# Kernel tuning notes

Measured on AMD Instinct MI355X. Metric: run time of the kernel, lower is better.

The kernel has to match this reference:

```python
import jax, jax.numpy as jnp
import numpy as np

N_NODES = 50000
N_EDGES = 800000
N_GRAPHS = 2048
F = 78  # num_features_xd


def gcn_conv(x, src, dst, W, b):
    """PyG GCNConv: x' = D^{-1/2}(A+I)D^{-1/2} (x W) + b, self-loops added."""
    n = x.shape[0]
    xw = x @ W  # dense transform first (PyG order)
    loop = jnp.arange(n)
    s = jnp.concatenate([src, loop])
    d = jnp.concatenate([dst, loop])
    deg = jax.ops.segment_sum(jnp.ones(d.shape[0], dtype=xw.dtype), d, num_segments=n)
    dis = jnp.where(deg > 0, jax.lax.rsqrt(deg), 0.0)
    norm = dis[s] * dis[d]  # [E+N]
    msg = xw[s] * norm[:, None]  # gather + scale, [E+N, Fout]
    out = jax.ops.segment_sum(msg, d, num_segments=n)  # scatter-add to targets
    return out + b


def setup_inputs() -> dict:
    key = jax.random.key(0)
    ks = jax.random.split(key, 9)

    def glorot(k, shape):
        lim = float(np.sqrt(6.0 / (shape[0] + shape[1])))
        return jax.random.uniform(k, shape, minval=-lim, maxval=lim, dtype=jnp.float32)

    x = jax.random.normal(ks[0], (N_NODES, F), dtype=jnp.float32)
    edge_index = jax.random.randint(ks[1], (2, N_EDGES), 0, N_NODES, dtype=jnp.int64)
    batch = jnp.sort(jax.random.randint(ks[2], (N_NODES,), 0, N_GRAPHS, dtype=jnp.int64))
    drug2 = jax.random.normal(ks[3], (N_GRAPHS, 489), dtype=jnp.float32)

    W1 = glorot(ks[4], (F, F));        b1 = jnp.zeros((F,), jnp.float32)
    W2 = glorot(ks[5], (F, 2 * F));    b2 = jnp.zeros((2 * F,), jnp.float32)
    W3 = glorot(ks[6], (2 * F, 4 * F)); b3 = jnp.zeros((4 * F,), jnp.float32)
    Wfc = glorot(ks[7], (4 * F, 489)); bfc = jnp.zeros((489,), jnp.float32)

    return dict(x=x, edge_index=edge_index, batch=batch, drug2=drug2,
                W1=W1, b1=b1, W2=W2, b2=b2, W3=W3, b3=b3, Wfc=Wfc, bfc=bfc)


def reference(x, edge_index, batch, drug2, W1, b1, W2, b2, W3, b3, Wfc, bfc):
    src, dst = edge_index[0], edge_index[1]
    h = jax.nn.relu(gcn_conv(x, src, dst, W1, b1))   # dropout = identity (eval mode)
    h = jax.nn.relu(gcn_conv(h, src, dst, W2, b2))
    h = jax.nn.relu(gcn_conv(h, src, dst, W3, b3))
    g = jax.ops.segment_max(h, batch, num_segments=N_GRAPHS)  # global max pool
    g = jnp.where(jnp.isfinite(g), g, 0.0)  # guard empty graphs
    g = jax.nn.relu(g @ Wfc + bfc)
    return g + drug2
```

## Files before the change

kernel.cpp:

```cpp
#include <hip/hip_runtime.h>

#define NNODES 50000
#define NEDGES 800000
#define NGRAPHS 2048

typedef __attribute__((ext_vector_type(8))) short bf16x8;
typedef __attribute__((ext_vector_type(4))) float f32x4;

__device__ __forceinline__ float bf2f(ushort u) {
    return __uint_as_float(((uint)u) << 16);
}
__device__ __forceinline__ ushort f2bf(float f) {
    uint u = __float_as_uint(f);
    return (ushort)((u + 0x7fff + ((u >> 16) & 1)) >> 16);
}

__global__ void deg_count(const int* __restrict__ dst, int* __restrict__ cnt, int E) {
    int e = blockIdx.x * blockDim.x + threadIdx.x;
    if (e < E) atomicAdd(&cnt[dst[e]], 1);
}

__global__ void block_scan(const int* __restrict__ cnt, int* __restrict__ lp,
                           int* __restrict__ bsum, int M) {
    __shared__ int s[256];
    int t = threadIdx.x;
    int n = blockIdx.x * 256 + t;
    int v = (n < M) ? cnt[n] : 0;
    s[t] = v;
    __syncthreads();
    #pragma unroll
    for (int off = 1; off < 256; off <<= 1) {
        int u = (t >= off) ? s[t - off] : 0;
        __syncthreads();
        s[t] += u;
        __syncthreads();
    }
    if (n < M) lp[n] = s[t] - v;
    if (t == 255) bsum[blockIdx.x] = s[255];
}

__global__ void scan_bsum(int* __restrict__ bsum, int NB) {
    __shared__ int s[256];
    int t = threadIdx.x;
    int v = (t < NB) ? bsum[t] : 0;
    s[t] = v;
    __syncthreads();
    #pragma unroll
    for (int off = 1; off < 256; off <<= 1) {
        int u = (t >= off) ? s[t - off] : 0;
        __syncthreads();
        s[t] += u;
        __syncthreads();
    }
    if (t < NB) bsum[t] = s[t] - v;
}

__global__ void finalize_rowptr(int* __restrict__ rowptr, int* __restrict__ cursor,
                                const int* __restrict__ bsum, const int* __restrict__ cnt,
                                float* __restrict__ dis,
                                const int* __restrict__ batch, int* __restrict__ gstart,
                                int M, int E, int G) {
    int n = blockIdx.x * blockDim.x + threadIdx.x;
    if (n < M) {
        int v = rowptr[n] + bsum[n >> 8];
        rowptr[n] = v;
        cursor[n] = v;
        dis[n] = rsqrtf((float)(cnt[n] + 1));
        int b = batch[n];
        int bp = (n == 0) ? -1 : batch[n - 1];
        for (int gg = bp + 1; gg <= b; ++gg) gstart[gg] = n;
        if (n == M - 1) {
            for (int gg = b + 1; gg <= G; ++gg) gstart[gg] = M;
        }
    }
    if (n == 0) rowptr[M] = E;
}

__global__ void fill_csr(const int* __restrict__ src, const int* __restrict__ dst,
                         const float* __restrict__ dis, int* __restrict__ cursor,
                         int2* __restrict__ csr, int E) {
    int e = blockIdx.x * blockDim.x + threadIdx.x;
    if (e >= E) return;
    int s = src[e], d = dst[e];
    int pos = atomicAdd(&cursor[d], 1);
    csr[pos] = make_int2(s, __float_as_int(dis[s] * dis[d]));
}

__global__ void prep_all(const float* __restrict__ x, ushort* __restrict__ xb,
                         const float* __restrict__ W1, ushort* __restrict__ W1t,
                         const float* __restrict__ W2, ushort* __restrict__ W2t,
                         const float* __restrict__ W3, ushort* __restrict__ W3t,
                         const float* __restrict__ Wfc, ushort* __restrict__ Wfct) {
    const int M = NNODES;
    const int KX = 80, F1 = 78, F2 = 156, F3 = 312, FC = 489;
    const int n0 = M * KX;
    const int n1 = 80 * 96, n2 = 160 * 96, n3 = 320 * 160, n4 = 496 * 320;
    int idx = blockIdx.x * blockDim.x + threadIdx.x;
    if (idx < n0) {
        int n = idx / KX, k = idx % KX;
        xb[idx] = (k < F1) ? f2bf(x[(size_t)n * F1 + k]) : (ushort)0;
        return;
    }
    idx -= n0;
    if (idx < n1) {
        int n = idx / 96, k = idx % 96;
        W1t[idx] = (k < F1 && n < F1) ? f2bf(W1[(size_t)k * F1 + n]) : (ushort)0;
        return;
    }
    idx -= n1;
    if (idx < n2) {
        int n = idx / 96, k = idx % 96;
        W2t[idx] = (k < F1 && n < F2) ? f2bf(W2[(size_t)k * F2 + n]) : (ushort)0;
        return;
    }
    idx -= n2;
    if (idx < n3) {
        int n = idx / 160, k = idx % 160;
        W3t[idx] = (k < F2 && n < F3) ? f2bf(W3[(size_t)k * F3 + n]) : (ushort)0;
        return;
    }
    idx -= n3;
    if (idx < n4) {
        int n = idx / 320, k = idx % 320;
        Wfct[idx] = (k < F3 && n < FC) ? f2bf(Wfc[(size_t)k * FC + n]) : (ushort)0;
    }
}

__device__ __forceinline__ void acc8(float* acc, uint4 v, float nm) {
    acc[0] += bf2f((ushort)(v.x & 0xffff)) * nm;
    acc[1] += bf2f((ushort)(v.x >> 16)) * nm;
    acc[2] += bf2f((ushort)(v.y & 0xffff)) * nm;
    acc[3] += bf2f((ushort)(v.y >> 16)) * nm;
    acc[4] += bf2f((ushort)(v.z & 0xffff)) * nm;
    acc[5] += bf2f((ushort)(v.z >> 16)) * nm;
    acc[6] += bf2f((ushort)(v.w & 0xffff)) * nm;
    acc[7] += bf2f((ushort)(v.w >> 16)) * nm;
}

template <int CH, int STR, int SUB, int CHOUT>
__global__ __launch_bounds__(128) void gather_ilp(const uint4* __restrict__ h,
                                                  const int* __restrict__ rowptr,
                                                  const int2* __restrict__ csr,
                                                  const float* __restrict__ dis,
                                                  uint4* __restrict__ agg) {
    int node = blockIdx.x * 2 + (threadIdx.x >> 6);
    if (node >= NNODES) return;
    int lane = threadIdx.x & 63;
    int sub = lane / CH;
    int ch = lane % CH;
    bool active = sub < SUB;

    float acc[8] = {};
    int beg = rowptr[node], end = rowptr[node + 1];
    for (int i = beg; i < end; i += 4 * SUB) {
        int2 ev[4];
        int vld[4];
        #pragma unroll
        for (int u = 0; u < 4; ++u) {
            int e = i + u * SUB + sub;
            vld[u] = active && (e < end);
            ev[u] = vld[u] ? csr[e] : make_int2(0, 0);
        }
        uint4 av[4];
        #pragma unroll
        for (int u = 0; u < 4; ++u)
            av[u] = vld[u] ? h[(size_t)ev[u].x * STR + ch] : make_uint4(0, 0, 0, 0);
        #pragma unroll
        for (int u = 0; u < 4; ++u)
            acc8(acc, av[u], __int_as_float(ev[u].y));
    }

    float tot[8];
    #pragma unroll
    for (int j = 0; j < 8; ++j) tot[j] = acc[j];
    #pragma unroll
    for (int sb = 1; sb < SUB; ++sb) {
        int srcLane = ch + sb * CH;
        #pragma unroll
        for (int j = 0; j < 8; ++j) tot[j] += __shfl(acc[j], srcLane);
    }

    if (lane < CHOUT) {
        uint4 o = make_uint4(0, 0, 0, 0);
        if (lane < CH) {
            float di = dis[node];
            float d2 = di * di;
            uint4 hs = h[(size_t)node * STR + lane];
            tot[0] += bf2f((ushort)(hs.x & 0xffff)) * d2;
            tot[1] += bf2f((ushort)(hs.x >> 16)) * d2;
            tot[2] += bf2f((ushort)(hs.y & 0xffff)) * d2;
            tot[3] += bf2f((ushort)(hs.y >> 16)) * d2;
            tot[4] += bf2f((ushort)(hs.z & 0xffff)) * d2;
            tot[5] += bf2f((ushort)(hs.z >> 16)) * d2;
            tot[6] += bf2f((ushort)(hs.w & 0xffff)) * d2;
            tot[7] += bf2f((ushort)(hs.w >> 16)) * d2;
            o.x = (uint)f2bf(tot[0]) | ((uint)f2bf(tot[1]) << 16);
            o.y = (uint)f2bf(tot[2]) | ((uint)f2bf(tot[3]) << 16);
            o.z = (uint)f2bf(tot[4]) | ((uint)f2bf(tot[5]) << 16);
            o.w = (uint)f2bf(tot[6]) | ((uint)f2bf(tot[7]) << 16);
        }
        agg[(size_t)node * CHOUT + lane] = o;
    }
}

template <int EPI>
__global__ __launch_bounds__(256) void gemm_mfma(const ushort* __restrict__ A,
                                                 const ushort* __restrict__ Bt,
                                                 ushort* __restrict__ Cb,
                                                 float* __restrict__ Cf,
                                                 const float* __restrict__ bias,
                                                 const float* __restrict__ addend,
                                                 int M, int Kp, int Np, int Nreal, int Cld) {
    __shared__ ushort Asl[64 * 32];
    __shared__ ushort Bsl[64 * 32];
    const int tid = threadIdx.x;
    const int lane = tid & 63;
    const int wid = tid >> 6;
    const int wm = (wid >> 1) * 32, wn = (wid & 1) * 32;
    const int bm = blockIdx.x * 64, bn = blockIdx.y * 64;

    const int sr = tid >> 2;
    const int sc = tid & 3;
    const int swz = sc ^ ((sr >> 1) & 3);
    const int lc = lane >> 4;

    f32x4 acc[2][2] = {};
    for (int k0 = 0; k0 < Kp; k0 += 32) {
        bf16x8 av = {};
        int gr = bm + sr;
        if (gr < M) av = *(const bf16x8*)&A[(size_t)gr * Kp + k0 + sc * 8];
        *(bf16x8*)&Asl[sr * 32 + swz * 8] = av;
        bf16x8 bv = {};
        int gn = bn + sr;
        if (gn < Np) bv = *(const bf16x8*)&Bt[(size_t)gn * Kp + k0 + sc * 8];
        *(bf16x8*)&Bsl[sr * 32 + swz * 8] = bv;
        __syncthreads();
        bf16x8 af[2], bfr[2];
        #pragma unroll
        for (int m = 0; m < 2; ++m) {
            int r = wm + m * 16 + (lane & 15);
            int pc = lc ^ ((r >> 1) & 3);
            af[m] = *(const bf16x8*)&Asl[r * 32 + pc * 8];
        }
        #pragma unroll
        for (int n = 0; n < 2; ++n) {
            int r = wn + n * 16 + (lane & 15);
            int pc = lc ^ ((r >> 1) & 3);
            bfr[n] = *(const bf16x8*)&Bsl[r * 32 + pc * 8];
        }
        #pragma unroll
        for (int m = 0; m < 2; ++m)
            #pragma unroll
            for (int n = 0; n < 2; ++n)
                acc[m][n] = __builtin_amdgcn_mfma_f32_16x16x32_bf16(af[m], bfr[n], acc[m][n], 0, 0, 0);
        __syncthreads();
    }
    #pragma unroll
    for (int m = 0; m < 2; ++m) {
        #pragma unroll
        for (int n = 0; n < 2; ++n) {
            int gc = bn + wn + n * 16 + (lane & 15);
            #pragma unroll
            for (int j = 0; j < 4; ++j) {
                int gr = bm + wm + m * 16 + (lane >> 4) * 4 + j;
                if (gr >= M) continue;
                float v = acc[m][n][j];
                if (EPI == 0) {
                    if (gc < Np) {
                        float o = (gc < Nreal) ? fmaxf(v + bias[gc], 0.f) : 0.f;
                        Cb[(size_t)gr * Cld + gc] = f2bf(o);
                    }
                } else {
                    if (gc < Nreal) {
                        float o = fmaxf(v + bias[gc], 0.f) + addend[(size_t)gr * Nreal + gc];
                        Cf[(size_t)gr * Nreal + gc] = o;
                    }
                }
            }
        }
    }
}

__global__ void pool_max_seg(const uint* __restrict__ h3, const int* __restrict__ gstart,
                             uint* __restrict__ gb, int PAIRS) {
    int g = blockIdx.x;
    int s = gstart[g], e = gstart[g + 1];
    for (int p = threadIdx.x; p < PAIRS; p += blockDim.x) {
        float mL = 0.f, mH = 0.f;
        for (int n = s; n < e; ++n) {
            uint v = h3[(size_t)n * PAIRS + p];
            mL = fmaxf(mL, bf2f((ushort)(v & 0xffff)));
            mH = fmaxf(mH, bf2f((ushort)(v >> 16)));
        }
        gb[(size_t)g * PAIRS + p] = (uint)f2bf(mL) | ((uint)f2bf(mH) << 16);
    }
}

extern "C" void kernel_launch(void* const* d_in, const int* in_sizes, int n_in,
                              void* d_out, int out_size, void* d_ws, size_t ws_size,
                              hipStream_t stream) {
    const float* x     = (const float*)d_in[0];
    const int*   eidx  = (const int*)d_in[1];
    const int*   batch = (const int*)d_in[2];
    const float* drug2 = (const float*)d_in[3];
    const float* W1 = (const float*)d_in[4];
    const float* b1 = (const float*)d_in[5];
    const float* W2 = (const float*)d_in[6];
    const float* b2 = (const float*)d_in[7];
    const float* W3 = (const float*)d_in[8];
    const float* b3 = (const float*)d_in[9];
    const float* Wfc = (const float*)d_in[10];
    const float* bfc = (const float*)d_in[11];
    float* out = (float*)d_out;

    const int M = NNODES, E = NEDGES, G = NGRAPHS;
    const int F1 = 78, F2 = 156, F3 = 312, FC = 489;
    const int Kx = 80;
    const int Kp1 = 96, Np1 = 80;
    const int Kp2 = 96, Np2 = 160;
    const int Kp3 = 160, Np3 = 320;
    const int Kpf = 320, Npf = 496;
    const int S2 = 192;

    const int* src = eidx;
    const int* dst = eidx + E;
    const int NB = (M + 255) / 256;

    char* ws = (char*)d_ws;
    size_t off = 0;
    auto alloc = [&](size_t bytes) {
        void* p = ws + off;
        off += (bytes + 255) & ~(size_t)255;
        return p;
    };
    ushort* xb   = (ushort*)alloc((size_t)M * Kx * 2);
    ushort* h1   = (ushort*)alloc((size_t)M * Np1 * 2);
    ushort* h2   = (ushort*)alloc((size_t)M * S2 * 2);
    ushort* h3   = (ushort*)alloc((size_t)M * Np3 * 2);
    ushort* agg  = (ushort*)alloc((size_t)M * Kp3 * 2);
    ushort* W1t  = (ushort*)alloc((size_t)Np1 * Kp1 * 2);
    ushort* W2t  = (ushort*)alloc((size_t)Np2 * Kp2 * 2);
    ushort* W3t  = (ushort*)alloc((size_t)Np3 * Kp3 * 2);
    ushort* Wfct = (ushort*)alloc((size_t)Npf * Kpf * 2);
    ushort* gb   = (ushort*)alloc((size_t)G * Kpf * 2);
    float* dis    = (float*)alloc((size_t)M * 4);
    int*   cnt    = (int*)alloc((size_t)M * 4);
    int*   rowptr = (int*)alloc((size_t)(M + 1) * 4);
    int*   cursor = (int*)alloc((size_t)M * 4);
    int*   bsum   = (int*)alloc(1024);
    int2*  csr    = (int2*)alloc((size_t)E * 8);
    int*   gstart  = (int*)alloc((size_t)(G + 1) * 4);

    hipMemsetAsync(cnt, 0, (size_t)M * 4, stream);
    deg_count<<<(E + 255) / 256, 256, 0, stream>>>(dst, cnt, E);
    block_scan<<<NB, 256, 0, stream>>>(cnt, rowptr, bsum, M);
    scan_bsum<<<1, 256, 0, stream>>>(bsum, NB);
    finalize_rowptr<<<NB, 256, 0, stream>>>(rowptr, cursor, bsum, cnt, dis, batch, gstart, M, E, G);
    fill_csr<<<(E + 255) / 256, 256, 0, stream>>>(src, dst, dis, cursor, csr, E);

    {
        int total = M * Kx + 80 * 96 + 160 * 96 + 320 * 160 + 496 * 320;
        prep_all<<<(total + 255) / 256, 256, 0, stream>>>(x, xb, W1, W1t, W2, W2t, W3, W3t, Wfc, Wfct);
    }

    const int GG = (M + 1) / 2;
    const int GMX = (M + 63) / 64;

    gather_ilp<10, 10, 6, 12><<<GG, 128, 0, stream>>>((const uint4*)xb, rowptr, csr, dis, (uint4*)agg);
    gemm_mfma<0><<<dim3(GMX, (Np1 + 63) / 64), 256, 0, stream>>>(agg, W1t, h1, nullptr, b1, nullptr, M, Kp1, Np1, F1, Np1);

    gather_ilp<10, 10, 6, 12><<<GG, 128, 0, stream>>>((const uint4*)h1, rowptr, csr, dis, (uint4*)agg);
    gemm_mfma<0><<<dim3(GMX, (Np2 + 63) / 64), 256, 0, stream>>>(agg, W2t, h2, nullptr, b2, nullptr, M, Kp2, Np2, F2, S2);

    gather_ilp<20, 24, 3, 20><<<GG, 128, 0, stream>>>((const uint4*)h2, rowptr, csr, dis, (uint4*)agg);
    gemm_mfma<0><<<dim3(GMX, Np3 / 64), 256, 0, stream>>>(agg, W3t, h3, nullptr, b3, nullptr, M, Kp3, Np3, F3, Np3);

    pool_max_seg<<<G, 256, 0, stream>>>((const uint*)h3, gstart, (uint*)gb, Kpf / 2);

    gemm_mfma<1><<<dim3((G + 63) / 64, (Npf + 63) / 64), 256, 0, stream>>>(gb, Wfct, nullptr, out, bfc, drug2, G, Kpf, Npf, FC, 0);
}
```

Measured before the change: 285.3 us.

## Build CSR via two-level bucket sort and compute edge norms on the fly

Replaces the global-atomic degree count, three-kernel scan and atomic CSR fill with a chunked histogram, bucket scan, shared-memory staged scatter into 256-node buckets, and a per-bucket local counting sort that also writes rowptr and dis. The CSR now stores only source indices, and the gather recomputes the edge norm from dis[src]*dis[node], which halves index traffic but adds a random dis load per edge. It also folds the graph-start computation into the prep kernel and shrinks the h2 row stride from 192 to 160. The point is to reduce global atomic contention and the number of small launches in graph preprocessing. Buckets above the shared capacity fall back to direct global writes.

```diff
diff --git a/kernel.cpp b/kernel.cpp
--- a/kernel.cpp
+++ b/kernel.cpp
@@ -3,6 +3,10 @@
 #define NNODES 50000
 #define NEDGES 800000
 #define NGRAPHS 2048
+#define CHUNK 4096
+#define NCHUNK ((NEDGES + CHUNK - 1) / CHUNK)
+#define NBUCK ((NNODES + 255) / 256)
+#define BCAP 4600
 
 typedef __attribute__((ext_vector_type(8))) short bf16x8;
 typedef __attribute__((ext_vector_type(4))) float f32x4;
@@ -15,82 +19,136 @@
     return (ushort)((u + 0x7fff + ((u >> 16) & 1)) >> 16);
 }
 
-__global__ void deg_count(const int* __restrict__ dst, int* __restrict__ cnt, int E) {
-    int e = blockIdx.x * blockDim.x + threadIdx.x;
-    if (e < E) atomicAdd(&cnt[dst[e]], 1);
-}
-
-__global__ void block_scan(const int* __restrict__ cnt, int* __restrict__ lp,
-                           int* __restrict__ bsum, int M) {
-    __shared__ int s[256];
+__global__ __launch_bounds__(256) void hist_pass(const int* __restrict__ dst,
+                                                 int* __restrict__ blockhist) {
+    __shared__ int bins[NBUCK];
+    int blk = blockIdx.x;
+    for (int i = threadIdx.x; i < NBUCK; i += 256) bins[i] = 0;
+    __syncthreads();
+    int e0 = blk * CHUNK;
+    int e1 = min(e0 + CHUNK, NEDGES);
+    for (int e = e0 + threadIdx.x; e < e1; e += 256)
+        atomicAdd(&bins[dst[e] >> 8], 1);
+    __syncthreads();
+    for (int i = threadIdx.x; i < NBUCK; i += 256)
+        blockhist[blk * NBUCK + i] = bins[i];
+}
+
+__global__ void bucket_scan(const int* __restrict__ blockhist,
+                            int* __restrict__ bucket_base,
+                            int* __restrict__ bucket_cursor) {
+    __shared__ int size_s[NBUCK];
+    for (int b = threadIdx.x; b < NBUCK; b += 256) {
+        int s = 0;
+        for (int c = 0; c < NCHUNK; ++c) s += blockhist[c * NBUCK + b];
+        size_s[b] = s;
+    }
+    __syncthreads();
+    if (threadIdx.x == 0) {
+        int run = 0;
+        for (int b = 0; b < NBUCK; ++b) { int v = size_s[b]; size_s[b] = run; run += v; }
+    }
+    __syncthreads();
+    for (int b = threadIdx.x; b < NBUCK; b += 256) {
+        bucket_base[b] = size_s[b];
+        bucket_cursor[b] = size_s[b];
+    }
+    if (threadIdx.x == 0) bucket_base[NBUCK] = NEDGES;
+}
+
+__global__ __launch_bounds__(256) void scatter_pass(const int* __restrict__ src,
+                                                    const int* __restrict__ dst,
+                                                    int* __restrict__ bucket_cursor,
+                                                    int2* __restrict__ ebuf) {
+    __shared__ int bins[NBUCK];
+    __shared__ int loff[NBUCK];
+    __shared__ int gbase[NBUCK];
+    __shared__ int lcur[NBUCK];
+    __shared__ int2 stage[CHUNK];
+    __shared__ int gaddr[CHUNK];
+    int blk = blockIdx.x;
+    int e0 = blk * CHUNK;
+    int e1 = min(e0 + CHUNK, NEDGES);
+    for (int i = threadIdx.x; i < NBUCK; i += 256) { bins[i] = 0; lcur[i] = 0; }
+    __syncthreads();
+    for (int e = e0 + threadIdx.x; e < e1; e += 256)
+        atomicAdd(&bins[dst[e] >> 8], 1);
+    __syncthreads();
+    if (threadIdx.x == 0) {
+        int run = 0;
+        for (int b = 0; b < NBUCK; ++b) { loff[b] = run; run += bins[b]; }
+    }
+    __syncthreads();
+    for (int b = threadIdx.x; b < NBUCK; b += 256)
+        gbase[b] = bins[b] ? atomicAdd(&bucket_cursor[b], bins[b]) : 0;
+    __syncthreads();
+    for (int e = e0 + threadIdx.x; e < e1; e += 256) {
+        int d = dst[e];
+        int b = d >> 8;
+        int p = atomicAdd(&lcur[b], 1);
+        int slot = loff[b] + p;
+        stage[slot] = make_int2(src[e], d);
+        gaddr[slot] = gbase[b] + p;
+    }
+    __syncthreads();
+    int cnt = e1 - e0;
+    for (int i = threadIdx.x; i < cnt; i += 256)
+        ebuf[gaddr[i]] = stage[i];
+}
+
+__global__ __launch_bounds__(256) void bucket_sort(const int2* __restrict__ ebuf,
+                                                   const int* __restrict__ bucket_base,
+                                                   int* __restrict__ csr_src,
+                                                   int* __restrict__ rowptr,
+                                                   float* __restrict__ dis) {
+    __shared__ int h[256], sc[257], cur[256];
+    __shared__ int srcstage[BCAP];
+    int b = blockIdx.x;
+    int base = bucket_base[b];
+    int cnt = bucket_base[b + 1] - base;
     int t = threadIdx.x;
-    int n = blockIdx.x * 256 + t;
-    int v = (n < M) ? cnt[n] : 0;
-    s[t] = v;
-    __syncthreads();
-    #pragma unroll
-    for (int off = 1; off < 256; off <<= 1) {
-        int u = (t >= off) ? s[t - off] : 0;
+    h[t] = 0;
+    cur[t] = 0;
+    __syncthreads();
+    for (int i = t; i < cnt; i += 256)
+        atomicAdd(&h[ebuf[base + i].y & 255], 1);
+    __syncthreads();
+    if (t == 0) {
+        int run = 0;
+        for (int j = 0; j < 256; ++j) { sc[j] = run; run += h[j]; }
+        sc[256] = run;
+    }
+    __syncthreads();
+    int node = b * 256 + t;
+    if (node <= NNODES) rowptr[node] = base + sc[t];
+    if (node < NNODES) dis[node] = rsqrtf((float)(h[t] + 1));
+    __syncthreads();
+    if (cnt <= BCAP) {
+        for (int i = t; i < cnt; i += 256) {
+            int2 r = ebuf[base + i];
+            int j = r.y & 255;
+            int p = atomicAdd(&cur[j], 1);
+            srcstage[sc[j] + p] = r.x;
+        }
         __syncthreads();
-        s[t] += u;
-        __syncthreads();
-    }
-    if (n < M) lp[n] = s[t] - v;
-    if (t == 255) bsum[blockIdx.x] = s[255];
-}
-
-__global__ void scan_bsum(int* __restrict__ bsum, int NB) {
-    __shared__ int s[256];
-    int t = threadIdx.x;
-    int v = (t < NB) ? bsum[t] : 0;
-    s[t] = v;
-    __syncthreads();
-    #pragma unroll
-    for (int off = 1; off < 256; off <<= 1) {
-        int u = (t >= off) ? s[t - off] : 0;
-        __syncthreads();
-        s[t] += u;
-        __syncthreads();
-    }
-    if (t < NB) bsum[t] = s[t] - v;
-}
-
-__global__ void finalize_rowptr(int* __restrict__ rowptr, int* __restrict__ cursor,
-                                const int* __restrict__ bsum, const int* __restrict__ cnt,
-                                float* __restrict__ dis,
-                                const int* __restrict__ batch, int* __restrict__ gstart,
-                                int M, int E, int G) {
-    int n = blockIdx.x * blockDim.x + threadIdx.x;
-    if (n < M) {
-        int v = rowptr[n] + bsum[n >> 8];
-        rowptr[n] = v;
-        cursor[n] = v;
-        dis[n] = rsqrtf((float)(cnt[n] + 1));
-        int b = batch[n];
-        int bp = (n == 0) ? -1 : batch[n - 1];
-        for (int gg = bp + 1; gg <= b; ++gg) gstart[gg] = n;
-        if (n == M - 1) {
-            for (int gg = b + 1; gg <= G; ++gg) gstart[gg] = M;
-        }
-    }
-    if (n == 0) rowptr[M] = E;
-}
-
-__global__ void fill_csr(const int* __restrict__ src, const int* __restrict__ dst,
-                         const float* __restrict__ dis, int* __restrict__ cursor,
-                         int2* __restrict__ csr, int E) {
-    int e = blockIdx.x * blockDim.x + threadIdx.x;
-    if (e >= E) return;
-    int s = src[e], d = dst[e];
-    int pos = atomicAdd(&cursor[d], 1);
-    csr[pos] = make_int2(s, __float_as_int(dis[s] * dis[d]));
+        for (int i = t; i < cnt; i += 256)
+            csr_src[base + i] = srcstage[i];
+    } else {
+        for (int i = t; i < cnt; i += 256) {
+            int2 r = ebuf[base + i];
+            int j = r.y & 255;
+            int p = atomicAdd(&cur[j], 1);
+            csr_src[base + sc[j] + p] = r.x;
+        }
+    }
 }
 
 __global__ void prep_all(const float* __restrict__ x, ushort* __restrict__ xb,
                          const float* __restrict__ W1, ushort* __restrict__ W1t,
                          const float* __restrict__ W2, ushort* __restrict__ W2t,
                          const float* __restrict__ W3, ushort* __restrict__ W3t,
-                         const float* __restrict__ Wfc, ushort* __restrict__ Wfct) {
+                         const float* __restrict__ Wfc, ushort* __restrict__ Wfct,
+                         const int* __restrict__ batch, int* __restrict__ gstart) {
     const int M = NNODES;
     const int KX = 80, F1 = 78, F2 = 156, F3 = 312, FC = 489;
     const int n0 = M * KX;
@@ -123,6 +181,17 @@
     if (idx < n4) {
         int n = idx / 320, k = idx % 320;
         Wfct[idx] = (k < F3 && n < FC) ? f2bf(Wfc[(size_t)k * FC + n]) : (ushort)0;
+        return;
+    }
+    idx -= n4;
+    if (idx < M) {
+        int n = idx;
+        int b = batch[n];
+        int bp = (n == 0) ? -1 : batch[n - 1];
+        for (int gg = bp + 1; gg <= b; ++gg) gstart[gg] = n;
+        if (n == M - 1) {
+            for (int gg = b + 1; gg <= NGRAPHS; ++gg) gstart[gg] = M;
+        }
     }
 }
 
@@ -140,7 +209,7 @@
 template <int CH, int STR, int SUB, int CHOUT>
 __global__ __launch_bounds__(128) void gather_ilp(const uint4* __restrict__ h,
                                                   const int* __restrict__ rowptr,
-                                                  const int2* __restrict__ csr,
+                                                  const int* __restrict__ csr_src,
                                                   const float* __restrict__ dis,
                                                   uint4* __restrict__ agg) {
     int node = blockIdx.x * 2 + (threadIdx.x >> 6);
@@ -149,25 +218,29 @@
     int sub = lane / CH;
     int ch = lane % CH;
     bool active = sub < SUB;
+    float di = dis[node];
 
     float acc[8] = {};
     int beg = rowptr[node], end = rowptr[node + 1];
     for (int i = beg; i < end; i += 4 * SUB) {
-        int2 ev[4];
+        int sidx[4];
         int vld[4];
         #pragma unroll
         for (int u = 0; u < 4; ++u) {
             int e = i + u * SUB + sub;
             vld[u] = active && (e < end);
-            ev[u] = vld[u] ? csr[e] : make_int2(0, 0);
+            sidx[u] = vld[u] ? csr_src[e] : 0;
         }
         uint4 av[4];
+        float ds[4];
+        #pragma unroll
+        for (int u = 0; u < 4; ++u) {
+            av[u] = vld[u] ? h[(size_t)sidx[u] * STR + ch] : make_uint4(0, 0, 0, 0);
+            ds[u] = dis[sidx[u]];
+        }
         #pragma unroll
         for (int u = 0; u < 4; ++u)
-            av[u] = vld[u] ? h[(size_t)ev[u].x * STR + ch] : make_uint4(0, 0, 0, 0);
-        #pragma unroll
-        for (int u = 0; u < 4; ++u)
-            acc8(acc, av[u], __int_as_float(ev[u].y));
+            acc8(acc, av[u], ds[u] * di);
     }
 
     float tot[8];
@@ -183,7 +256,6 @@
     if (lane < CHOUT) {
         uint4 o = make_uint4(0, 0, 0, 0);
         if (lane < CH) {
-            float di = dis[node];
             float d2 = di * di;
             uint4 hs = h[(size_t)node * STR + lane];
             tot[0] += bf2f((ushort)(hs.x & 0xffff)) * d2;
@@ -320,11 +392,9 @@
     const int Kp2 = 96, Np2 = 160;
     const int Kp3 = 160, Np3 = 320;
     const int Kpf = 320, Npf = 496;
-    const int S2 = 192;
 
     const int* src = eidx;
     const int* dst = eidx + E;
-    const int NB = (M + 255) / 256;
 
     char* ws = (char*)d_ws;
     size_t off = 0;
@@ -335,7 +405,7 @@
     };
     ushort* xb   = (ushort*)alloc((size_t)M * Kx * 2);
     ushort* h1   = (ushort*)alloc((size_t)M * Np1 * 2);
-    ushort* h2   = (ushort*)alloc((size_t)M * S2 * 2);
+    ushort* h2   = (ushort*)alloc((size_t)M * Np2 * 2);
     ushort* h3   = (ushort*)alloc((size_t)M * Np3 * 2);
     ushort* agg  = (ushort*)alloc((size_t)M * Kp3 * 2);
     ushort* W1t  = (ushort*)alloc((size_t)Np1 * Kp1 * 2);
@@ -344,38 +414,39 @@
     ushort* Wfct = (ushort*)alloc((size_t)Npf * Kpf * 2);
     ushort* gb   = (ushort*)alloc((size_t)G * Kpf * 2);
     float* dis    = (float*)alloc((size_t)M * 4);
-    int*   cnt    = (int*)alloc((size_t)M * 4);
     int*   rowptr = (int*)alloc((size_t)(M + 1) * 4);
-    int*   cursor = (int*)alloc((size_t)M * 4);
-    int*   bsum   = (int*)alloc(1024);
-    int2*  csr    = (int2*)alloc((size_t)E * 8);
-    int*   gstart  = (int*)alloc((size_t)(G + 1) * 4);
-
-    hipMemsetAsync(cnt, 0, (size_t)M * 4, stream);
-    deg_count<<<(E + 255) / 256, 256, 0, stream>>>(dst, cnt, E);
-    block_scan<<<NB, 256, 0, stream>>>(cnt, rowptr, bsum, M);
-    scan_bsum<<<1, 256, 0, stream>>>(bsum, NB);
-    finalize_rowptr<<<NB, 256, 0, stream>>>(rowptr, cursor, bsum, cnt, dis, batch, gstart, M, E, G);
-    fill_csr<<<(E + 255) / 256, 256, 0, stream>>>(src, dst, dis, cursor, csr, E);
+    int2*  ebuf   = (int2*)alloc((size_t)E * 8);
+    int*   csr_src = (int*)alloc((size_t)E * 4);
+    int*   blockhist = (int*)alloc((size_t)NCHUNK * NBUCK * 4);
+    int*   bucket_base = (int*)alloc((size_t)(NBUCK + 1) * 4);
+    int*   bucket_cursor = (int*)alloc((size_t)NBUCK * 4);
+    int*   gstart = (int*)alloc((size_t)(G + 1) * 4);
 
     {
-        int total = M * Kx + 80 * 96 + 160 * 96 + 320 * 160 + 496 * 320;
-        prep_all<<<(total + 255) / 256, 256, 0, stream>>>(x, xb, W1, W1t, W2, W2t, W3, W3t, Wfc, Wfct);
-    }
+        int total = M * Kx + 80 * 96 + 160 * 96 + 320 * 160 + 496 * 320 + M;
+        prep_all<<<(total + 255) / 256, 256, 0, stream>>>(
+            x, xb, W1, W1t, W2, W2t, W3, W3t, Wfc, Wfct, batch, gstart);
+    }
+
+    hist_pass<<<NCHUNK, 256, 0, stream>>>(dst, blockhist);
+    bucket_scan<<<1, 256, 0, stream>>>(blockhist, bucket_base, bucket_cursor);
+    scatter_pass<<<NCHUNK, 256, 0, stream>>>(src, dst, bucket_cursor, ebuf);
+    bucket_sort<<<NBUCK, 256, 0, stream>>>(ebuf, bucket_base, csr_src, rowptr, dis);
 
     const int GG = (M + 1) / 2;
     const int GMX = (M + 63) / 64;
 
-    gather_ilp<10, 10, 6, 12><<<GG, 128, 0, stream>>>((const uint4*)xb, rowptr, csr, dis, (uint4*)agg);
+    gather_ilp<10, 10, 6, 12><<<GG, 128, 0, stream>>>((const uint4*)xb, rowptr, csr_src, dis, (uint4*)agg);
     gemm_mfma<0><<<dim3(GMX, (Np1 + 63) / 64), 256, 0, stream>>>(agg, W1t, h1, nullptr, b1, nullptr, M, Kp1, Np1, F1, Np1);
 
-    gather_ilp<10, 10, 6, 12><<<GG, 128, 0, stream>>>((const uint4*)h1, rowptr, csr, dis, (uint4*)agg);
-    gemm_mfma<0><<<dim3(GMX, (Np2 + 63) / 64), 256, 0, stream>>>(agg, W2t, h2, nullptr, b2, nullptr, M, Kp2, Np2, F2, S2);
-
-    gather_ilp<20, 24, 3, 20><<<GG, 128, 0, stream>>>((const uint4*)h2, rowptr, csr, dis, (uint4*)agg);
+    gather_ilp<10, 10, 6, 12><<<GG, 128, 0, stream>>>((const uint4*)h1, rowptr, csr_src, dis, (uint4*)agg);
+    gemm_mfma<0><<<dim3(GMX, (Np2 + 63) / 64), 256, 0, stream>>>(agg, W2t, h2, nullptr, b2, nullptr, M, Kp2, Np2, F2, Np2);
+
+    gather_ilp<20, 20, 3, 20><<<GG, 128, 0, stream>>>((const uint4*)h2, rowptr, csr_src, dis, (uint4*)agg);
     gemm_mfma<0><<<dim3(GMX, Np3 / 64), 256, 0, stream>>>(agg, W3t, h3, nullptr, b3, nullptr, M, Kp3, Np3, F3, Np3);
 
     pool_max_seg<<<G, 256, 0, stream>>>((const uint*)h3, gstart, (uint*)gb, Kpf / 2);
 
-    gemm_mfma<1><<<dim3((G + 63) / 64, (Npf + 63) / 64), 256, 0, stream>>>(gb, Wfct, nullptr, out, bfc, drug2, G, Kpf, Npf, FC, 0);
-}
+    gemm_mfma<1><<<dim3((G + 63) / 64, (Npf + 63) / 64), 256, 0, stream>>>(
+        gb, Wfct, nullptr, out, bfc, drug2, G, Kpf, Npf, FC, 0);
+}
```

Result: faster. 235.2 us, median of 2 (-17.6%).
